# Optimization experiments

Hardware: AMD Instinct MI355X
Metric: run time of the kernel (lower is better)

Reference implementation:

```python
import jax, jax.numpy as jnp
import numpy as np

DIM = 768
HID = 3072
HID2 = HID // 2
MAX_LEVEL = 8
N_LEV = MAX_LEVEL + 1
BATCH, SEQ = 2, 2048
EPS = 1e-5


def _layernorm(x, gamma, beta):
    m = jnp.mean(x, axis=-1, keepdims=True)
    v = jnp.mean(jnp.square(x - m), axis=-1, keepdims=True)
    return (x - m) * jax.lax.rsqrt(v + EPS) * gamma + beta


def setup_inputs() -> dict:
    key = jax.random.key(0)
    ks = jax.random.split(key, 12)
    s = 0.02
    return {
        "x": jax.random.normal(ks[0], (BATCH, SEQ, DIM), dtype=jnp.float32),
        "levels_info": jax.random.randint(ks[1], (SEQ, 4), 0, N_LEV, dtype=jnp.int32),
        "gamma": jnp.ones((DIM,), dtype=jnp.float32),
        "beta": jnp.zeros((DIM,), dtype=jnp.float32),
        "W1": jax.random.normal(ks[2], (DIM, HID), dtype=jnp.float32) * s,
        "b1": jnp.zeros((HID,), dtype=jnp.float32),
        "W2": jax.random.normal(ks[3], (HID, DIM), dtype=jnp.float32) * s,
        "b2": jnp.zeros((DIM,), dtype=jnp.float32),
        "A1": jax.random.normal(ks[4], (N_LEV, DIM, HID2), dtype=jnp.float32) * s,
        "a1b": jnp.zeros((N_LEV, HID2), dtype=jnp.float32),
        "A2": jax.random.normal(ks[5], (N_LEV, HID2, DIM), dtype=jnp.float32) * s,
        "a2b": jnp.zeros((N_LEV, DIM), dtype=jnp.float32),
        "lmw": jnp.ones((N_LEV,), dtype=jnp.float32)
        + jax.random.normal(ks[6], (N_LEV,), dtype=jnp.float32) * 0.1,
    }


def reference(x, levels_info, gamma, beta, W1, b1, W2, b2, A1, a1b, A2, a2b, lmw):
    # x: [B,S,D]
    x_norm = _layernorm(x, gamma, beta)
    # main MLP: Linear -> GELU (exact, torch default) -> Linear; dropout=0 is identity
    h = jax.nn.gelu(jnp.einsum("bsd,dh->bsh", x_norm, W1) + b1, approximate=False)
    main_out = jnp.einsum("bsh,hd->bsd", h, W2) + b2

    # per-token depth-indexed adapter routing
    depths = jnp.clip(levels_info[:, 0], 0, MAX_LEVEL)  # [S]
    level_adapted = jnp.zeros_like(main_out)
    for lvl in range(N_LEV):  # small fixed expert set
        mask = (depths == lvl).astype(x.dtype)[None, :, None]  # [1,S,1]
        hl = jax.nn.relu(jnp.einsum("bsd,dh->bsh", x_norm, A1[lvl]) + a1b[lvl])
        level_adapted = level_adapted + mask * (
            jnp.einsum("bsh,hd->bsd", hl, A2[lvl]) + a2b[lvl]
        )

    # softmax over the sequence axis (faithful to F.softmax(..., dim=0))
    mix = jax.nn.softmax(lmw[depths], axis=0)[None, :, None]  # [1,S,1]
    return main_out * (1.0 - mix) + level_adapted * mix
```

## Files before the change

### kernel.cpp

```cpp
#include <hip/hip_runtime.h>
#include <hip/hip_bf16.h>
#include <math.h>

typedef __bf16 bf16;
typedef __bf16 bf16x4 __attribute__((ext_vector_type(4)));
typedef __bf16 bf16x8 __attribute__((ext_vector_type(8)));
typedef float f32x4 __attribute__((ext_vector_type(4)));

#define DIM 768
#define HID 3072
#define HID2 1536
#define NLEV 9
#define SEQ 2048
#define ROWS 4096
#define MAXPAD 5248
#define MAXTILES 41

__device__ __forceinline__ void gld16(const void* g, void* l) {
    __builtin_amdgcn_global_load_lds(
        (const __attribute__((address_space(1))) void*)g,
        (__attribute__((address_space(3))) void*)l, 16, 0, 0);
}

__device__ __forceinline__ float fast_gelu(float v) {
    float v2 = v * v;
    float twou = v * (1.59576912f + 0.071354816f * v2);
    float t = __expf(twou);
    return v * t / (t + 1.0f);
}


__device__ __forceinline__ void ln4_body(int blk,
                                         const float* __restrict__ x,
                                         const float* __restrict__ gamma,
                                         const float* __restrict__ beta,
                                         bf16* __restrict__ xn) {
    int tid = threadIdx.x;
    int wv = tid >> 6, ln = tid & 63;
    int row = blk * 4 + wv;
    const float* xr = x + (size_t)row * DIM;
    int c = ln * 4;
    float4 v0 = *(const float4*)(xr + c);
    float4 v1 = *(const float4*)(xr + c + 256);
    float4 v2 = *(const float4*)(xr + c + 512);
    float s = v0.x + v0.y + v0.z + v0.w
            + v1.x + v1.y + v1.z + v1.w
            + v2.x + v2.y + v2.z + v2.w;
    float q = v0.x * v0.x + v0.y * v0.y + v0.z * v0.z + v0.w * v0.w
            + v1.x * v1.x + v1.y * v1.y + v1.z * v1.z + v1.w * v1.w
            + v2.x * v2.x + v2.y * v2.y + v2.z * v2.z + v2.w * v2.w;
#pragma unroll
    for (int off = 32; off; off >>= 1) {
        s += __shfl_xor(s, off, 64);
        q += __shfl_xor(q, off, 64);
    }
    float m = s * (1.0f / DIM);
    float r = rsqrtf(q * (1.0f / DIM) - m * m + 1e-5f);
    bf16* xo = xn + (size_t)row * DIM;
#pragma unroll
    for (int p = 0; p < 3; p++) {
        int cc = c + p * 256;
        float4 v = (p == 0) ? v0 : (p == 1) ? v1 : v2;
        float4 g = *(const float4*)(gamma + cc);
        float4 b = *(const float4*)(beta + cc);
        bf16x4 o;
        o[0] = (bf16)((v.x - m) * r * g.x + b.x);
        o[1] = (bf16)((v.y - m) * r * g.y + b.y);
        o[2] = (bf16)((v.z - m) * r * g.z + b.z);
        o[3] = (bf16)((v.w - m) * r * g.w + b.w);
        *(bf16x4*)(xo + cc) = o;
    }
}

__device__ __forceinline__ void transpose_body64(float* sm,
                                                 const float* __restrict__ inb,
                                                 bf16* __restrict__ outb,
                                                 int R, int C, int bx, int by) {
    int tid = threadIdx.x;
    int ty = tid >> 4;
    int tx4 = (tid & 15) * 4;
#pragma unroll
    for (int p = 0; p < 4; p++) {
        int rloc = p * 16 + ty;
        int row = by * 64 + rloc;
        float4 v = *(const float4*)(inb + (size_t)row * C + bx * 64 + tx4);
        sm[rloc * 65 + tx4 + 0] = v.x;
        sm[rloc * 65 + tx4 + 1] = v.y;
        sm[rloc * 65 + tx4 + 2] = v.z;
        sm[rloc * 65 + tx4 + 3] = v.w;
    }
    __syncthreads();
    int ch = tid & 7;
    int ocb = tid >> 3;
#pragma unroll
    for (int p = 0; p < 2; p++) {
        int oc = p * 32 + ocb;
        bf16x8 tmp;
#pragma unroll
        for (int k = 0; k < 8; k++) tmp[k] = (bf16)sm[(ch * 8 + k) * 65 + oc];
        *(bf16x8*)(outb + (size_t)(bx * 64 + oc) * R + by * 64 + ch * 8) = tmp;
    }
}

__device__ __forceinline__ void routing_body(float* sm,
                                             const int* __restrict__ levels_info,
                                             const float* __restrict__ lmw,
                                             float* __restrict__ mix,
                                             int* __restrict__ row_index,
                                             int* __restrict__ tile_meta,
                                             float* __restrict__ zbuf) {
    int* cnt = (int*)sm;
    int* cur = cnt + NLEV;
    int* off = cur + NLEV;
    float* mixv = (float*)(off + NLEV);
    int tid = threadIdx.x;
    if (tid < NLEV) { cnt[tid] = 0; cur[tid] = 0; }
    __syncthreads();
    for (int s = tid; s < SEQ; s += 256) {
        int d = levels_info[s * 4];
        d = d < 0 ? 0 : (d > 8 ? 8 : d);
        atomicAdd(&cnt[d], 1);
    }
    for (int i = tid; i < MAXPAD; i += 256) row_index[i] = -1;
    for (int i = tid; i < 512; i += 256) zbuf[i] = 0.0f;
    __syncthreads();
    if (tid == 0) {
        float mx = lmw[0];
        for (int l = 1; l < NLEV; l++) mx = fmaxf(mx, lmw[l]);
        float denom = 0.f;
        for (int l = 0; l < NLEV; l++) denom += (float)cnt[l] * expf(lmw[l] - mx);
        float inv = 1.0f / denom;
        int running = 0, t = 0;
        for (int l = 0; l < NLEV; l++) {
            mixv[l] = expf(lmw[l] - mx) * inv;
            off[l] = running;
            int seg = (2 * cnt[l] + 127) & ~127;
            for (int k = 0; k < seg / 128; k++) tile_meta[t++] = l;
            running += seg;
        }
        for (; t < MAXTILES; t++) tile_meta[t] = -1;
    }
    __syncthreads();
    for (int s = tid; s < SEQ; s += 256) {
        int d = levels_info[s * 4];
        d = d < 0 ? 0 : (d > 8 ? 8 : d);
        int p = atomicAdd(&cur[d], 2);
        row_index[off[d] + p]     = s;
        row_index[off[d] + p + 1] = s + SEQ;
        mix[s] = mixv[d];
    }
}

__global__ __launch_bounds__(256) void prep_kernel(const float* __restrict__ x,
                                                   const int* __restrict__ levels_info,
                                                   const float* __restrict__ gamma,
                                                   const float* __restrict__ beta,
                                                   const float* __restrict__ W1,
                                                   const float* __restrict__ A1,
                                                   const float* __restrict__ lmw,
                                                   bf16* __restrict__ Xn,
                                                   bf16* __restrict__ W1t,
                                                   bf16* __restrict__ A1t,
                                                   float* __restrict__ mix,
                                                   int* __restrict__ row_index,
                                                   int* __restrict__ tile_meta,
                                                   float* __restrict__ zbuf) {
    __shared__ __align__(16) float sm[64 * 65];
    int b = blockIdx.x;
    if (b == 0) { routing_body(sm, levels_info, lmw, mix, row_index, tile_meta, zbuf); return; }
    int i = b - 1;
    int tb;
    if (i < 4096) {
        if ((i & 3) == 0) { ln4_body(i >> 2, x, gamma, beta, Xn); return; }
        tb = (i >> 2) * 3 + (i & 3) - 1;
    } else {
        tb = 3072 + (i - 4096);
    }
    if (tb < 576) {
        transpose_body64(sm, W1, W1t, DIM, HID, tb % 48, tb / 48);
        return;
    }
    tb -= 576;
    {
        int bz = tb / 288, r = tb % 288;
        transpose_body64(sm, A1 + (size_t)bz * DIM * HID2, A1t + (size_t)bz * DIM * HID2,
                         DIM, HID2, r % 24, r / 24);
    }
}

template<int KT>
__device__ __forceinline__ void gemm_loop_db(const bf16* ga0, const bf16* ga1,
                                             const bf16* gb0, const bf16* gb1,
                                             bf16* As, bf16* Bs,
                                             f32x4 (&acc)[4][4]) {
    int tid = threadIdx.x;
    int wv = tid >> 6;
    int lane = tid & 63;
    int wm = wv >> 1, wn = wv & 1;
    int swz = (lane >> 1) & 3;
    int achunk = ((lane >> 4) ^ swz) * 8;
    int aoff = ((wm * 64) + (lane & 15)) * 32 + achunk;
    int boff = ((wn * 64) + (lane & 15)) * 32 + achunk;
    gld16(ga0, As + wv * 512);
    gld16(ga1, As + 2048 + wv * 512);
    gld16(gb0, Bs + wv * 512);
    gld16(gb1, Bs + 2048 + wv * 512);
    ga0 += 32; ga1 += 32; gb0 += 32; gb1 += 32;
#pragma unroll
    for (int kt = 0; kt < KT; ++kt) {
        __syncthreads();
        const int cur = (kt & 1) << 12;
        const int nxt = cur ^ 4096;
        if (kt + 1 < KT) {
            gld16(ga0, As + nxt + wv * 512);
            gld16(ga1, As + nxt + 2048 + wv * 512);
            gld16(gb0, Bs + nxt + wv * 512);
            gld16(gb1, Bs + nxt + 2048 + wv * 512);
            ga0 += 32; ga1 += 32; gb0 += 32; gb1 += 32;
        }
        bf16x8 af[4], bfr[4];
#pragma unroll
        for (int i = 0; i < 4; i++) af[i] = *(const bf16x8*)(As + cur + aoff + i * 512);
#pragma unroll
        for (int j = 0; j < 4; j++) bfr[j] = *(const bf16x8*)(Bs + cur + boff + j * 512);
#pragma unroll
        for (int i = 0; i < 4; i++)
#pragma unroll
            for (int j = 0; j < 4; j++)
                acc[i][j] = __builtin_amdgcn_mfma_f32_16x16x32_bf16(af[i], bfr[j], acc[i][j], 0, 0, 0);
    }
}

#define ACC_INIT(acc) \
    _Pragma("unroll") for (int i = 0; i < 4; i++) \
    _Pragma("unroll") for (int j = 0; j < 4; j++) acc[i][j] = (f32x4){0.f, 0.f, 0.f, 0.f};

#define SWZ_CG(tid) (((tid) & 3) ^ (((tid) >> 3) & 3))

__device__ __forceinline__ void store_tile(const bf16* cbuf, int lane,
                                           bf16* gptr, int ldg) {
#pragma unroll
    for (int p = 0; p < 8; p++) {
        int lrow = p * 8 + (lane >> 3);
        int chunk = (lane & 7) * 8;
        bf16x8 v = *(const bf16x8*)(cbuf + lrow * 64 + chunk);
        *(bf16x8*)(gptr + (size_t)lrow * ldg + chunk) = v;
    }
}

__global__ __launch_bounds__(256) void mlp1_kernel(const bf16* __restrict__ Xn,
                                                   const bf16* __restrict__ W1t,
                                                   const float* __restrict__ b1,
                                                   bf16* __restrict__ H,
                                                   const bf16* __restrict__ A1t,
                                                   const float* __restrict__ a1b,
                                                   const int* __restrict__ row_index,
                                                   const int* __restrict__ tile_meta,
                                                   const bf16* __restrict__ zbuf,
                                                   bf16* __restrict__ HL,
                                                   const float* __restrict__ W2,
                                                   const float* __restrict__ A2,
                                                   bf16* __restrict__ W2t,
                                                   bf16* __restrict__ A2t) {
    __shared__ __align__(16) bf16 smem[16384];
    bf16* As = smem;
    bf16* Bs = smem + 8192;
    int b = blockIdx.x;
    int bid = (b < 2520) ? ((b & 1) ? (1260 + (b >> 1)) : (b >> 1)) : b;
    int tid = threadIdx.x;
    int r0 = tid >> 2, cg = SWZ_CG(tid);
    int lane = tid & 63, wv = tid >> 6, wm = wv >> 1, wn = wv & 1;
    bf16* cbuf = smem + wv * 4096;

    if (bid < 768) {
        int nb = bid / 32, mb = bid % 32;
        f32x4 acc[4][4];
        ACC_INIT(acc);
        const bf16* ga0 = Xn + (size_t)(mb * 128 + r0) * DIM + cg * 8;
        const bf16* ga1 = ga0 + (size_t)64 * DIM;
        const bf16* gb0 = W1t + (size_t)(nb * 128 + r0) * DIM + cg * 8;
        const bf16* gb1 = gb0 + (size_t)64 * DIM;
        gemm_loop_db<24>(ga0, ga1, gb0, gb1, As, Bs, acc);
        int cbase = nb * 128 + wn * 64 + (lane & 15);
        __syncthreads();
#pragma unroll
        for (int j = 0; j < 4; j++) {
            float bias = b1[cbase + j * 16];
#pragma unroll
            for (int i = 0; i < 4; i++)
#pragma unroll
                for (int r = 0; r < 4; r++) {
                    int lrow = i * 16 + ((lane >> 4) << 2) + r;
                    int lcol = j * 16 + (lane & 15);
                    cbuf[lrow * 64 + lcol] = (bf16)fast_gelu(acc[i][j][r] + bias);
                }
        }
        __syncthreads();
        store_tile(cbuf, lane, H + (size_t)(mb * 128 + wm * 64) * HID + nb * 128 + wn * 64, HID);
    } else if (bid < 1260) {
        int t2 = bid - 768;
        int nb = t2 % 12, t = t2 / 12;
        int lvl = tile_meta[t];
        if (lvl < 0) return;
        f32x4 acc[4][4];
        ACC_INIT(acc);
        int ridx0 = row_index[t * 128 + r0];
        int ridx1 = row_index[t * 128 + 64 + r0];
        const bf16* ga0 = (ridx0 >= 0) ? (Xn + (size_t)ridx0 * DIM + cg * 8) : (zbuf + cg * 8);
        const bf16* ga1 = (ridx1 >= 0) ? (Xn + (size_t)ridx1 * DIM + cg * 8) : (zbuf + cg * 8);
        const bf16* Bl = A1t + (size_t)lvl * HID2 * DIM;
        const bf16* gb0 = Bl + (size_t)(nb * 128 + r0) * DIM + cg * 8;
        const bf16* gb1 = gb0 + (size_t)64 * DIM;
        gemm_loop_db<24>(ga0, ga1, gb0, gb1, As, Bs, acc);
        int cbase = nb * 128 + wn * 64 + (lane & 15);
        __syncthreads();
#pragma unroll
        for (int j = 0; j < 4; j++) {
            float bias = a1b[lvl * HID2 + cbase + j * 16];
#pragma unroll
            for (int i = 0; i < 4; i++)
#pragma unroll
                for (int r = 0; r < 4; r++) {
                    int lrow = i * 16 + ((lane >> 4) << 2) + r;
                    int lcol = j * 16 + (lane & 15);
                    cbuf[lrow * 64 + lcol] = (bf16)fmaxf(acc[i][j][r] + bias, 0.0f);
                }
        }
        __syncthreads();
        store_tile(cbuf, lane, HL + (size_t)(t * 128 + wm * 64) * HID2 + nb * 128 + wn * 64, HID2);
    } else if (bid < 1836) {
        int idx = bid - 1260;
        transpose_body64((float*)smem, W2, W2t, HID, DIM, idx % 12, idx / 12);
    } else {
        int idx = bid - 1836;
        int bz = idx / 288, r = idx % 288;
        transpose_body64((float*)smem, A2 + (size_t)bz * HID2 * DIM,
                         A2t + (size_t)bz * HID2 * DIM, HID2, DIM, r % 12, r / 12);
    }
}

__global__ __launch_bounds__(256) void mlp2_kernel(const bf16* __restrict__ H,
                                                   const bf16* __restrict__ W2t,
                                                   bf16* __restrict__ part,
                                                   const bf16* __restrict__ HL,
                                                   const bf16* __restrict__ A2t,
                                                   const float* __restrict__ a2b,
                                                   const int* __restrict__ row_index,
                                                   const int* __restrict__ tile_meta,
                                                   bf16* __restrict__ apart) {
    __shared__ __align__(16) bf16 smem[16384];
    bf16* As = smem;
    bf16* Bs = smem + 8192;
    int bid = blockIdx.x, tid = threadIdx.x;
    int r0 = tid >> 2, cg = SWZ_CG(tid);
    int lane = tid & 63, wv = tid >> 6, wm = wv >> 1, wn = wv & 1;
    bf16* cbuf = smem + wv * 4096;
    f32x4 acc[4][4];
    ACC_INIT(acc);

    if (bid < 384) {
        int cc = bid % 12;
        int nb = cc >> 1, ks = cc & 1;
        int mb = bid / 12;
        const bf16* ga0 = H + (size_t)(mb * 128 + r0) * HID + ks * 1536 + cg * 8;
        const bf16* ga1 = ga0 + (size_t)64 * HID;
        const bf16* gb0 = W2t + (size_t)(nb * 128 + r0) * HID + ks * 1536 + cg * 8;
        const bf16* gb1 = gb0 + (size_t)64 * HID;
        gemm_loop_db<48>(ga0, ga1, gb0, gb1, As, Bs, acc);
        __syncthreads();
#pragma unroll
        for (int j = 0; j < 4; j++)
#pragma unroll
            for (int i = 0; i < 4; i++)
#pragma unroll
                for (int r = 0; r < 4; r++) {
                    int lrow = i * 16 + ((lane >> 4) << 2) + r;
                    int lcol = j * 16 + (lane & 15);
                    cbuf[lrow * 64 + lcol] = (bf16)acc[i][j][r];
                }
        __syncthreads();
        bf16* pk = part + (size_t)ks * ROWS * DIM;
        store_tile(cbuf, lane, pk + (size_t)(mb * 128 + wm * 64) * DIM + nb * 128 + wn * 64, DIM);
    } else {
        int t2 = bid - 384;
        int nb = t2 % 6, t = t2 / 6;
        int lvl = tile_meta[t];
        if (lvl < 0) return;
        const bf16* ga0 = HL + (size_t)(t * 128 + r0) * HID2 + cg * 8;
        const bf16* ga1 = ga0 + (size_t)64 * HID2;
        const bf16* Bl = A2t + (size_t)lvl * DIM * HID2;
        const bf16* gb0 = Bl + (size_t)(nb * 128 + r0) * HID2 + cg * 8;
        const bf16* gb1 = gb0 + (size_t)64 * HID2;
        gemm_loop_db<48>(ga0, ga1, gb0, gb1, As, Bs, acc);
        int cbase = nb * 128 + wn * 64 + (lane & 15);
        __syncthreads();
#pragma unroll
        for (int j = 0; j < 4; j++) {
            float bias = a2b[lvl * DIM + cbase + j * 16];
#pragma unroll
            for (int i = 0; i < 4; i++)
#pragma unroll
                for (int r = 0; r < 4; r++) {
                    int lrow = i * 16 + ((lane >> 4) << 2) + r;
                    int lcol = j * 16 + (lane & 15);
                    cbuf[lrow * 64 + lcol] = (bf16)(acc[i][j][r] + bias);
                }
        }
        __syncthreads();
        int colg = nb * 128 + wn * 64;
#pragma unroll
        for (int p = 0; p < 8; p++) {
            int lrow = p * 8 + (lane >> 3);
            int chunk = (lane & 7) * 8;
            int rg = row_index[t * 128 + wm * 64 + lrow];
            if (rg >= 0) {
                bf16x8 v = *(const bf16x8*)(cbuf + lrow * 64 + chunk);
                *(bf16x8*)(apart + (size_t)rg * DIM + colg + chunk) = v;
            }
        }
    }
}

__global__ __launch_bounds__(256) void combine_kernel(const bf16* __restrict__ part,
                                                      const bf16* __restrict__ apart,
                                                      const float* __restrict__ b2,
                                                      const float* __restrict__ mix,
                                                      float* __restrict__ out) {
    int i = blockIdx.x * 256 + threadIdx.x;
    int base = i * 4;
    int row = base / DIM;
    int c = base - row * DIM;
    float mx = mix[row & (SEQ - 1)];
    bf16x4 p0 = *(const bf16x4*)(part + base);
    bf16x4 p1 = *(const bf16x4*)(part + (size_t)ROWS * DIM + base);
    bf16x4 a0 = *(const bf16x4*)(apart + base);
    float4 o;
    float* po = &o.x;
#pragma unroll
    for (int k = 0; k < 4; k++) {
        float main_v = (float)p0[k] + (float)p1[k] + b2[c + k];
        po[k] = (1.0f - mx) * main_v + mx * (float)a0[k];
    }
    *(float4*)(out + base) = o;
}

extern "C" void kernel_launch(void* const* d_in, const int* in_sizes, int n_in,
                              void* d_out, int out_size, void* d_ws, size_t ws_size,
                              hipStream_t stream) {
    const float* x    = (const float*)d_in[0];
    const int* levels = (const int*)d_in[1];
    const float* gamma= (const float*)d_in[2];
    const float* beta = (const float*)d_in[3];
    const float* W1   = (const float*)d_in[4];
    const float* b1   = (const float*)d_in[5];
    const float* W2   = (const float*)d_in[6];
    const float* b2   = (const float*)d_in[7];
    const float* A1   = (const float*)d_in[8];
    const float* a1b  = (const float*)d_in[9];
    const float* A2   = (const float*)d_in[10];
    const float* a2b  = (const float*)d_in[11];
    const float* lmw  = (const float*)d_in[12];
    float* out = (float*)d_out;

    char* p = (char*)d_ws;
    auto alloc = [&](size_t bytes) {
        char* r = p;
        p += (bytes + 255) & ~(size_t)255;
        return r;
    };
    bf16* Xn   = (bf16*)alloc((size_t)ROWS * DIM * 2);
    bf16* W1t  = (bf16*)alloc((size_t)HID * DIM * 2);
    bf16* W2t  = (bf16*)alloc((size_t)DIM * HID * 2);
    bf16* A1t  = (bf16*)alloc((size_t)NLEV * HID2 * DIM * 2);
    bf16* A2t  = (bf16*)alloc((size_t)NLEV * DIM * HID2 * 2);
    bf16* H    = (bf16*)alloc((size_t)ROWS * HID * 2);
    bf16* HL   = (bf16*)alloc((size_t)MAXPAD * HID2 * 2);
    bf16* part = (bf16*)alloc((size_t)2 * ROWS * DIM * 2);
    bf16* apart= (bf16*)alloc((size_t)ROWS * DIM * 2);
    float* mix = (float*)alloc(SEQ * 4);
    int* row_index = (int*)alloc(MAXPAD * 4);
    int* tile_meta = (int*)alloc(MAXTILES * 4);
    float* zbuf    = (float*)alloc(2048);

    prep_kernel<<<dim3(1 + 1024 + 576 + 2592), dim3(256), 0, stream>>>(
        x, levels, gamma, beta, W1, A1, lmw,
        Xn, W1t, A1t, mix, row_index, tile_meta, zbuf);

    mlp1_kernel<<<dim3(768 + 492 + 576 + 2592), dim3(256), 0, stream>>>(
        Xn, W1t, b1, H, A1t, a1b, row_index, tile_meta, (const bf16*)zbuf, HL,
        W2, A2, W2t, A2t);

    mlp2_kernel<<<dim3(384 + MAXTILES * 6), dim3(256), 0, stream>>>(
        H, W2t, part, HL, A2t, a2b, row_index, tile_meta, apart);

    combine_kernel<<<dim3(ROWS * DIM / 1024), dim3(256), 0, stream>>>(
        part, apart, b2, mix, out);
}
```

Before: 309.6 us.

## Move W2/A2 transposes into prep kernel and shrink transpose LDS to bf16

The W2 and A2 weight transposes move out of the first GEMM kernel and into the prep kernel, so the GEMM kernel launches only its GEMM tiles. The prep kernel's block mapping becomes sequential instead of interleaving layernorm with transpose blocks. The transpose staging buffer now holds bf16 with a stride of 68, which halves LDS use and lets stores be vectorized. The trade-off is that the transposes no longer overlap with GEMM work, and the prep kernel grows longer and now sits on the critical path.

```diff
diff --git a/kernel.cpp b/kernel.cpp
--- a/kernel.cpp
+++ b/kernel.cpp
@@ -72,7 +72,7 @@
     }
 }
 
-__device__ __forceinline__ void transpose_body64(float* sm,
+__device__ __forceinline__ void transpose_body64(bf16* sm,
                                                  const float* __restrict__ inb,
                                                  bf16* __restrict__ outb,
                                                  int R, int C, int bx, int by) {
@@ -84,10 +84,9 @@
         int rloc = p * 16 + ty;
         int row = by * 64 + rloc;
         float4 v = *(const float4*)(inb + (size_t)row * C + bx * 64 + tx4);
-        sm[rloc * 65 + tx4 + 0] = v.x;
-        sm[rloc * 65 + tx4 + 1] = v.y;
-        sm[rloc * 65 + tx4 + 2] = v.z;
-        sm[rloc * 65 + tx4 + 3] = v.w;
+        bf16x4 o;
+        o[0] = (bf16)v.x; o[1] = (bf16)v.y; o[2] = (bf16)v.z; o[3] = (bf16)v.w;
+        *(bf16x4*)(sm + rloc * 68 + tx4) = o;
     }
     __syncthreads();
     int ch = tid & 7;
@@ -97,7 +96,7 @@
         int oc = p * 32 + ocb;
         bf16x8 tmp;
 #pragma unroll
-        for (int k = 0; k < 8; k++) tmp[k] = (bf16)sm[(ch * 8 + k) * 65 + oc];
+        for (int k = 0; k < 8; k++) tmp[k] = sm[(ch * 8 + k) * 68 + oc];
         *(bf16x8*)(outb + (size_t)(bx * 64 + oc) * R + by * 64 + ch * 8) = tmp;
     }
 }
@@ -157,34 +156,45 @@
                                                    const float* __restrict__ beta,
                                                    const float* __restrict__ W1,
                                                    const float* __restrict__ A1,
+                                                   const float* __restrict__ W2,
+                                                   const float* __restrict__ A2,
                                                    const float* __restrict__ lmw,
                                                    bf16* __restrict__ Xn,
                                                    bf16* __restrict__ W1t,
                                                    bf16* __restrict__ A1t,
+                                                   bf16* __restrict__ W2t,
+                                                   bf16* __restrict__ A2t,
                                                    float* __restrict__ mix,
                                                    int* __restrict__ row_index,
                                                    int* __restrict__ tile_meta,
                                                    float* __restrict__ zbuf) {
-    __shared__ __align__(16) float sm[64 * 65];
+    __shared__ __align__(16) bf16 tsm[64 * 68];
     int b = blockIdx.x;
-    if (b == 0) { routing_body(sm, levels_info, lmw, mix, row_index, tile_meta, zbuf); return; }
-    int i = b - 1;
-    int tb;
-    if (i < 4096) {
-        if ((i & 3) == 0) { ln4_body(i >> 2, x, gamma, beta, Xn); return; }
-        tb = (i >> 2) * 3 + (i & 3) - 1;
-    } else {
-        tb = 3072 + (i - 4096);
-    }
-    if (tb < 576) {
-        transpose_body64(sm, W1, W1t, DIM, HID, tb % 48, tb / 48);
+    if (b == 0) { routing_body((float*)tsm, levels_info, lmw, mix, row_index, tile_meta, zbuf); return; }
+    b -= 1;
+    if (b < 1024) { ln4_body(b, x, gamma, beta, Xn); return; }
+    b -= 1024;
+    if (b < 576) {
+        transpose_body64(tsm, W1, W1t, DIM, HID, b % 48, b / 48);
         return;
     }
-    tb -= 576;
+    b -= 576;
+    if (b < 2592) {
+        int bz = b / 288, r = b % 288;
+        transpose_body64(tsm, A1 + (size_t)bz * DIM * HID2, A1t + (size_t)bz * DIM * HID2,
+                         DIM, HID2, r % 24, r / 24);
+        return;
+    }
+    b -= 2592;
+    if (b < 576) {
+        transpose_body64(tsm, W2, W2t, HID, DIM, b % 12, b / 12);
+        return;
+    }
+    b -= 576;
     {
-        int bz = tb / 288, r = tb % 288;
-        transpose_body64(sm, A1 + (size_t)bz * DIM * HID2, A1t + (size_t)bz * DIM * HID2,
-                         DIM, HID2, r % 24, r / 24);
+        int bz = b / 288, r = b % 288;
+        transpose_body64(tsm, A2 + (size_t)bz * HID2 * DIM, A2t + (size_t)bz * HID2 * DIM,
+                         HID2, DIM, r % 12, r / 12);
     }
 }
 
@@ -257,17 +267,11 @@
                                                    const int* __restrict__ row_index,
                                                    const int* __restrict__ tile_meta,
                                                    const bf16* __restrict__ zbuf,
-                                                   bf16* __restrict__ HL,
-                                                   const float* __restrict__ W2,
-                                                   const float* __restrict__ A2,
-                                                   bf16* __restrict__ W2t,
-                                                   bf16* __restrict__ A2t) {
+                                                   bf16* __restrict__ HL) {
     __shared__ __align__(16) bf16 smem[16384];
     bf16* As = smem;
     bf16* Bs = smem + 8192;
-    int b = blockIdx.x;
-    int bid = (b < 2520) ? ((b & 1) ? (1260 + (b >> 1)) : (b >> 1)) : b;
-    int tid = threadIdx.x;
+    int bid = blockIdx.x, tid = threadIdx.x;
     int r0 = tid >> 2, cg = SWZ_CG(tid);
     int lane = tid & 63, wv = tid >> 6, wm = wv >> 1, wn = wv & 1;
     bf16* cbuf = smem + wv * 4096;
@@ -297,7 +301,7 @@
         }
         __syncthreads();
         store_tile(cbuf, lane, H + (size_t)(mb * 128 + wm * 64) * HID + nb * 128 + wn * 64, HID);
-    } else if (bid < 1260) {
+    } else {
         int t2 = bid - 768;
         int nb = t2 % 12, t = t2 / 12;
         int lvl = tile_meta[t];
@@ -328,14 +332,6 @@
         }
         __syncthreads();
         store_tile(cbuf, lane, HL + (size_t)(t * 128 + wm * 64) * HID2 + nb * 128 + wn * 64, HID2);
-    } else if (bid < 1836) {
-        int idx = bid - 1260;
-        transpose_body64((float*)smem, W2, W2t, HID, DIM, idx % 12, idx / 12);
-    } else {
-        int idx = bid - 1836;
-        int bz = idx / 288, r = idx % 288;
-        transpose_body64((float*)smem, A2 + (size_t)bz * HID2 * DIM,
-                         A2t + (size_t)bz * HID2 * DIM, HID2, DIM, r % 12, r / 12);
     }
 }
 
@@ -482,13 +478,12 @@
     int* tile_meta = (int*)alloc(MAXTILES * 4);
     float* zbuf    = (float*)alloc(2048);
 
-    prep_kernel<<<dim3(1 + 1024 + 576 + 2592), dim3(256), 0, stream>>>(
-        x, levels, gamma, beta, W1, A1, lmw,
-        Xn, W1t, A1t, mix, row_index, tile_meta, zbuf);
-
-    mlp1_kernel<<<dim3(768 + 492 + 576 + 2592), dim3(256), 0, stream>>>(
-        Xn, W1t, b1, H, A1t, a1b, row_index, tile_meta, (const bf16*)zbuf, HL,
-        W2, A2, W2t, A2t);
+    prep_kernel<<<dim3(1 + 1024 + 576 + 2592 + 576 + 2592), dim3(256), 0, stream>>>(
+        x, levels, gamma, beta, W1, A1, W2, A2, lmw,
+        Xn, W1t, A1t, W2t, A2t, mix, row_index, tile_meta, zbuf);
+
+    mlp1_kernel<<<dim3(768 + 492), dim3(256), 0, stream>>>(
+        Xn, W1t, b1, H, A1t, a1b, row_index, tile_meta, (const bf16*)zbuf, HL);
 
     mlp2_kernel<<<dim3(384 + MAXTILES * 6), dim3(256), 0, stream>>>(
         H, W2t, part, HL, A2t, a2b, row_index, tile_meta, apart);
```

New measurement: 280.6 us. 1.1x faster.
